# Performance work log

Measured on AMD Instinct MI355X. Metric: run time of the kernel, lower is better.

## Reference

```python
import jax, jax.numpy as jnp
import numpy as np

H, D, RPE_DIM, LAYERS = 8, 64, 64, 3
GAMMA = 0.999  # fixed decay (use_decay=True, requires_grad=False)
EPS = 1e-8

def simple_rmsnorm(x):
    # SimpleRMSNorm: x / (||x||_2 * d^{-1/2} + eps), no learned scale
    rms = jnp.sqrt(jnp.sum(x * x, axis=-1, keepdims=True)) * (x.shape[-1] ** -0.5)
    return x / (rms + EPS)

def rpe_transform(idx, pos_proj_w, pos_proj_b, layer_ws, layer_bs, out_w, out_b):
    # idx: (n, 1) -> (H, n, D)
    x = idx @ pos_proj_w + pos_proj_b            # (n, RPE_DIM)
    for i in range(LAYERS):                       # residual=False -> sequential
        x = jax.nn.relu(simple_rmsnorm(x)) @ layer_ws[i] + layer_bs[i]
    x = jax.nn.relu(simple_rmsnorm(x)) @ out_w + out_b   # (n, H*D)
    n = x.shape[0]
    return x.reshape(n, H, D).transpose(1, 0, 2)  # (H, n, D)

def setup_inputs() -> dict:
    key = jax.random.key(0)
    ks = jax.random.split(key, 6)
    b, n = 8, 4096
    s = RPE_DIM ** -0.5
    return {
        "x": jax.random.normal(ks[0], (b, H, n, D), jnp.float32),
        "pos_proj_w": jax.random.normal(ks[1], (1, RPE_DIM), jnp.float32),
        "pos_proj_b": jnp.zeros((RPE_DIM,), jnp.float32),
        "layer_ws": jax.random.normal(ks[2], (LAYERS, RPE_DIM, RPE_DIM), jnp.float32) * s,
        "layer_bs": jnp.zeros((LAYERS, RPE_DIM), jnp.float32),
        "out_w": jax.random.normal(ks[3], (RPE_DIM, H * D), jnp.float32) * s,
        "out_b": jnp.zeros((H * D,), jnp.float32),
    }

def reference(x, pos_proj_w, pos_proj_b, layer_ws, layer_bs, out_w, out_b):
    b, h, n, d = x.shape
    _rpe = lambda idx: rpe_transform(idx, pos_proj_w, pos_proj_b, layer_ws, layer_bs, out_w, out_b)
    # relative-position kernel values (par_type=1: raw integer offsets)
    zero = _rpe(jnp.zeros((1, 1), x.dtype))                       # (H, 1, D)
    pos_idx = jnp.arange(1, n, dtype=x.dtype).reshape(n - 1, 1)   # 1..n-1
    pos = _rpe(pos_idx)                                           # (H, n-1, D)
    neg = _rpe(-pos_idx[::-1])                                    # -(n-1)..-1
    # fixed exponential decay gamma^|offset|
    coef = jnp.arange(1, n, dtype=x.dtype).reshape(1, n - 1, 1)
    gamma = jnp.full((h, 1, d), GAMMA, x.dtype) ** coef           # (H, n-1, D)
    pos = gamma * pos
    neg = gamma[:, ::-1, :] * neg
    # act_type='none' -> identity activation on a
    a = jnp.concatenate([zero, pos, zero, neg], axis=1)           # (H, 2n, D)
    # circular conv of length 2n realizes the Toeplitz matvec
    y = jnp.fft.rfft(x, n=2 * n, axis=-2)                         # (b,H,n+1?,D) complex
    v = jnp.fft.rfft(a, n=2 * n, axis=-2)[None]                   # (1,H,.,D)
    out = jnp.fft.irfft(v * y, n=2 * n, axis=-2)[:, :, :n, :]
    return out
```

## Files before the change

kernel.cpp:

```cpp
#include <hip/hip_runtime.h>
#include <math.h>

#define NF 8192

__device__ __forceinline__ int phys(int e) { return e ^ (((e >> 4) & 7) << 1); }

__device__ __forceinline__ float2 cmul(float2 a, float2 b) {
    return make_float2(a.x*b.x - a.y*b.y, a.x*b.y + a.y*b.x);
}
__device__ __forceinline__ float2 cmulc(float2 a, float2 b) {
    return make_float2(a.x*b.x + a.y*b.y, a.y*b.x - a.x*b.y);
}
__device__ __forceinline__ float2 cadd(float2 a, float2 b){ return make_float2(a.x+b.x, a.y+b.y); }
__device__ __forceinline__ float2 csub(float2 a, float2 b){ return make_float2(a.x-b.x, a.y-b.y); }
__device__ __forceinline__ float2 mnegi(float2 a){ return make_float2(a.y, -a.x); }
__device__ __forceinline__ float2 mposi(float2 a){ return make_float2(-a.y, a.x); }
#define RSQ2 0.70710678118654752f
__device__ __forceinline__ float2 mw81 (float2 a){ return make_float2( RSQ2*(a.x+a.y),  RSQ2*(a.y-a.x)); }
__device__ __forceinline__ float2 mw83 (float2 a){ return make_float2( RSQ2*(a.y-a.x), -RSQ2*(a.x+a.y)); }
__device__ __forceinline__ float2 mw81c(float2 a){ return make_float2( RSQ2*(a.x-a.y),  RSQ2*(a.x+a.y)); }
__device__ __forceinline__ float2 mw83c(float2 a){ return make_float2(-RSQ2*(a.x+a.y),  RSQ2*(a.x-a.y)); }

#define C16_1 0.92387953251128674f
#define S16_1 0.38268343236508978f
#define C16_2 0.70710678118654752f

__device__ __forceinline__ float2 twbase(int ts) {
    float fa = (float)ts * (1.0f/8192.0f);
    return make_float2(__builtin_amdgcn_cosf(fa), -__builtin_amdgcn_sinf(fa));
}

__device__ __forceinline__ void dif8_core(float2& v0, float2& v1, float2& v2, float2& v3,
                                          float2& v4, float2& v5, float2& v6, float2& v7) {
    float2 t;
    t = csub(v0, v4); v0 = cadd(v0, v4); v4 = t;
    t = csub(v1, v5); v1 = cadd(v1, v5); v5 = mw81(t);
    t = csub(v2, v6); v2 = cadd(v2, v6); v6 = mnegi(t);
    t = csub(v3, v7); v3 = cadd(v3, v7); v7 = mw83(t);
    t = csub(v0, v2); v0 = cadd(v0, v2); v2 = t;
    t = csub(v1, v3); v1 = cadd(v1, v3); v3 = mnegi(t);
    t = csub(v4, v6); v4 = cadd(v4, v6); v6 = t;
    t = csub(v5, v7); v5 = cadd(v5, v7); v7 = mnegi(t);
    t = csub(v0, v1); v0 = cadd(v0, v1); v1 = t;
    t = csub(v2, v3); v2 = cadd(v2, v3); v3 = t;
    t = csub(v4, v5); v4 = cadd(v4, v5); v5 = t;
    t = csub(v6, v7); v6 = cadd(v6, v7); v7 = t;
}

__device__ __forceinline__ void dit8_core(float2& v0, float2& v1, float2& v2, float2& v3,
                                          float2& v4, float2& v5, float2& v6, float2& v7) {
    float2 t;
    t = csub(v0, v1); v0 = cadd(v0, v1); v1 = t;
    t = csub(v2, v3); v2 = cadd(v2, v3); v3 = t;
    t = csub(v4, v5); v4 = cadd(v4, v5); v5 = t;
    t = csub(v6, v7); v6 = cadd(v6, v7); v7 = t;
    t = v2;        v2 = csub(v0, t); v0 = cadd(v0, t);
    t = mposi(v3); v3 = csub(v1, t); v1 = cadd(v1, t);
    t = v6;        v6 = csub(v4, t); v4 = cadd(v4, t);
    t = mposi(v7); v7 = csub(v5, t); v5 = cadd(v5, t);
    t = v4;        v4 = csub(v0, t); v0 = cadd(v0, t);
    t = mw81c(v5); v5 = csub(v1, t); v1 = cadd(v1, t);
    t = mposi(v6); v6 = csub(v2, t); v2 = cadd(v2, t);
    t = mw83c(v7); v7 = csub(v3, t); v3 = cadd(v3, t);
}

#define TW_POWERS(ts) \
    float2 w1 = twbase(ts); \
    float2 w2 = cmul(w1, w1); \
    float2 w3 = cmul(w2, w1); \
    float2 w4 = cmul(w2, w2); \
    float2 w5 = cmul(w3, w2); \
    float2 w6 = cmul(w3, w3); \
    float2 w7 = cmul(w4, w3);

template<int M, int LM>
__device__ __forceinline__ void fwd8_lds(float2* Z, int tid) {
    #pragma unroll
    for (int q = 0; q < 2; ++q) {
        int beta = tid + q*512;
        int i    = beta & (M-1);
        int base = ((beta >> LM) << (LM+3)) + i;
        float2 v0 = Z[phys(base        )];
        float2 v1 = Z[phys(base + 1*M)];
        float2 v2 = Z[phys(base + 2*M)];
        float2 v3 = Z[phys(base + 3*M)];
        float2 v4 = Z[phys(base + 4*M)];
        float2 v5 = Z[phys(base + 5*M)];
        float2 v6 = Z[phys(base + 6*M)];
        float2 v7 = Z[phys(base + 7*M)];
        dif8_core(v0,v1,v2,v3,v4,v5,v6,v7);
        TW_POWERS((NF >> (LM+3)) * i)
        Z[phys(base        )] = v0;
        Z[phys(base + 4*M)] = cmul(v1, w4);
        Z[phys(base + 2*M)] = cmul(v2, w2);
        Z[phys(base + 6*M)] = cmul(v3, w6);
        Z[phys(base + 1*M)] = cmul(v4, w1);
        Z[phys(base + 5*M)] = cmul(v5, w5);
        Z[phys(base + 3*M)] = cmul(v6, w3);
        Z[phys(base + 7*M)] = cmul(v7, w7);
    }
}

template<int M, int LM>
__device__ __forceinline__ void inv8_lds(float2* Z, int tid) {
    #pragma unroll
    for (int q = 0; q < 2; ++q) {
        int beta = tid + q*512;
        int i    = beta & (M-1);
        int base = ((beta >> LM) << (LM+3)) + i;
        TW_POWERS((NF >> (LM+3)) * i)
        float2 v0 = Z[phys(base        )];
        float2 v1 = cmulc(Z[phys(base + 4*M)], w4);
        float2 v2 = cmulc(Z[phys(base + 2*M)], w2);
        float2 v3 = cmulc(Z[phys(base + 6*M)], w6);
        float2 v4 = cmulc(Z[phys(base + 1*M)], w1);
        float2 v5 = cmulc(Z[phys(base + 5*M)], w5);
        float2 v6 = cmulc(Z[phys(base + 3*M)], w3);
        float2 v7 = cmulc(Z[phys(base + 7*M)], w7);
        dit8_core(v0,v1,v2,v3,v4,v5,v6,v7);
        Z[phys(base        )] = v0;
        Z[phys(base + 1*M)] = v1;
        Z[phys(base + 2*M)] = v2;
        Z[phys(base + 3*M)] = v3;
        Z[phys(base + 4*M)] = v4;
        Z[phys(base + 5*M)] = v5;
        Z[phys(base + 6*M)] = v6;
        Z[phys(base + 7*M)] = v7;
    }
}


__global__ __launch_bounds__(512) void rpe_kernel(
    const float* __restrict__ pw,  const float* __restrict__ pb,
    const float* __restrict__ lws, const float* __restrict__ lbs,
    const float* __restrict__ ow,  const float* __restrict__ ob,
    float* __restrict__ a_buf)
{
    __shared__ float sW[3][64][64];
    __shared__ float sWo[64][64];
    __shared__ float sB[3][64];
    __shared__ float sPW[64], sPB[64];
    __shared__ float sAct[8][4][64];
    int tid = threadIdx.x;
    for (int idx = tid; idx < 3*64*64; idx += 512) ((float*)sW)[idx] = lws[idx];
    if (tid < 192) ((float*)sB)[tid] = lbs[tid];
    if (tid < 64) { sPW[tid] = pw[tid]; sPB[tid] = pb[tid]; }
    __syncthreads();

    int wv = tid >> 6, lane = tid & 63;
    int e0 = blockIdx.x * 32 + wv * 4;
    float dec[4];
    #pragma unroll
    for (int s = 0; s < 4; ++s) {
        int e = e0 + s;
        float p = (e == 4096) ? 0.f : ((e < 4096) ? (float)e : (float)(e - 8192));
        int m = (e < 4096) ? e : (8192 - e);
        if (e == 4096) m = 0;
        dec[s] = exp2f(-0.0014434309482562475f * (float)m);

        float xv = fmaf(p, sPW[lane], sPB[lane]);
        #pragma unroll
        for (int L = 0; L < 3; ++L) {
            float ss = xv * xv;
            #pragma unroll
            for (int o = 1; o < 64; o <<= 1) ss += __shfl_xor(ss, o);
            sAct[wv][s][lane] = fmaxf(xv / (sqrtf(ss) * 0.125f + 1e-8f), 0.f);
            float y = sB[L][lane];
            const float4* av = reinterpret_cast<const float4*>(sAct[wv][s]);
            #pragma unroll
            for (int k = 0; k < 16; ++k) {
                float4 a4 = av[k];
                y = fmaf(a4.x, sW[L][4*k  ][lane], y);
                y = fmaf(a4.y, sW[L][4*k+1][lane], y);
                y = fmaf(a4.z, sW[L][4*k+2][lane], y);
                y = fmaf(a4.w, sW[L][4*k+3][lane], y);
            }
            xv = y;
        }
        float ss = xv * xv;
        #pragma unroll
        for (int o = 1; o < 64; o <<= 1) ss += __shfl_xor(ss, o);
        sAct[wv][s][lane] = fmaxf(xv / (sqrtf(ss) * 0.125f + 1e-8f), 0.f);
    }
    for (int qq = 0; qq < 8; ++qq) {
        __syncthreads();
        for (int idx = tid; idx < 4096; idx += 512)
            ((float*)sWo)[idx] = ow[(size_t)(idx >> 6)*512 + qq*64 + (idx & 63)];
        __syncthreads();
        #pragma unroll
        for (int s = 0; s < 4; ++s) {
            float y = ob[qq*64 + lane];
            const float4* av = reinterpret_cast<const float4*>(sAct[wv][s]);
            #pragma unroll
            for (int k = 0; k < 16; ++k) {
                float4 a4 = av[k];
                y = fmaf(a4.x, sWo[4*k  ][lane], y);
                y = fmaf(a4.y, sWo[4*k+1][lane], y);
                y = fmaf(a4.z, sWo[4*k+2][lane], y);
                y = fmaf(a4.w, sWo[4*k+3][lane], y);
            }
            a_buf[(size_t)(qq*64 + lane)*NF + (e0 + s)] = y * dec[s];
        }
    }
}

__global__ __launch_bounds__(512, 4) void afft_kernel(
    const float* __restrict__ a_buf, float2* __restrict__ Afft)
{
    __shared__ __align__(16) float2 Z[NF];
    int cc = blockIdx.x, tid = threadIdx.x;
    const float* col = a_buf + (size_t)cc * NF;
    #pragma unroll
    for (int q = 0; q < 2; ++q) {
        int i = tid + q*512;
        float2 v0 = make_float2(col[i       ], 0.f);
        float2 v1 = make_float2(col[i + 1024], 0.f);
        float2 v2 = make_float2(col[i + 2048], 0.f);
        float2 v3 = make_float2(col[i + 3072], 0.f);
        float2 v4 = make_float2(col[i + 4096], 0.f);
        float2 v5 = make_float2(col[i + 5120], 0.f);
        float2 v6 = make_float2(col[i + 6144], 0.f);
        float2 v7 = make_float2(col[i + 7168], 0.f);
        dif8_core(v0,v1,v2,v3,v4,v5,v6,v7);
        TW_POWERS(i)
        Z[phys(i        )] = v0;
        Z[phys(i + 4096)] = cmul(v1, w4);
        Z[phys(i + 2048)] = cmul(v2, w2);
        Z[phys(i + 6144)] = cmul(v3, w6);
        Z[phys(i + 1024)] = cmul(v4, w1);
        Z[phys(i + 5120)] = cmul(v5, w5);
        Z[phys(i + 3072)] = cmul(v6, w3);
        Z[phys(i + 7168)] = cmul(v7, w7);
    }
    __syncthreads();
    fwd8_lds<128, 7>(Z, tid);  __syncthreads();
    fwd8_lds<16,  4>(Z, tid);  __syncthreads();
    {
        int c = tid, sw4 = c & 7;
        float4* Z4 = reinterpret_cast<float4*>(Z);
        float4* oc4 = reinterpret_cast<float4*>(Afft + (size_t)cc * NF);
        float2 z[16];
        #pragma unroll
        for (int j = 0; j < 8; ++j) {
            float4 wv = Z4[c*8 + (j ^ sw4)];
            z[2*j]   = make_float2(wv.x, wv.y);
            z[2*j+1] = make_float2(wv.z, wv.w);
        }
        dif8_core(z[0],z[2],z[4],z[6],z[8],z[10],z[12],z[14]);
        dif8_core(z[1],z[3],z[5],z[7],z[9],z[11],z[13],z[15]);
        #define A4K(k, ZE, ZO, WR, WI) { \
            float2 w = make_float2((WR)*(ZO).x - (WI)*(ZO).y, (WR)*(ZO).y + (WI)*(ZO).x); \
            float2 pp = cadd(ZE, w), rr = csub(ZE, w); \
            oc4[(k)*512 + c] = make_float4(pp.x, pp.y, rr.x, rr.y); }
        { float2 pp = cadd(z[0], z[1]), rr = csub(z[0], z[1]);
          oc4[0*512 + c] = make_float4(pp.x, pp.y, rr.x, rr.y); }
        A4K(1, z[8],  z[9],   C16_1, -S16_1)
        A4K(2, z[4],  z[5],   C16_2, -C16_2)
        A4K(3, z[12], z[13],  S16_1, -C16_1)
        { float2 w = mnegi(z[3]);
          float2 pp = cadd(z[2], w), rr = csub(z[2], w);
          oc4[4*512 + c] = make_float4(pp.x, pp.y, rr.x, rr.y); }
        A4K(5, z[10], z[11], -S16_1, -C16_1)
        A4K(6, z[6],  z[7],  -C16_2, -C16_2)
        A4K(7, z[14], z[15], -C16_1, -S16_1)
        #undef A4K
    }
}

__global__ __launch_bounds__(512, 4) void conv_kernel(
    const float* __restrict__ x, const float2* __restrict__ Afft,
    float* __restrict__ out)
{
    __shared__ __align__(16) float2 Z[NF];
    int blk = blockIdx.x;
    int c8 = blk & 7, r = blk >> 3;
    int d  = ((c8 & 1) << 5) | (r & 31);
    int h  = (((r >> 5) & 3) << 1) | ((c8 >> 1) & 1);
    int bp = (((r >> 7) & 1) << 1) | ((c8 >> 2) & 1);
    int tid = threadIdx.x;
    size_t base0 = ((size_t)((bp*2 + 0)*8 + h) * 4096) * 64 + d;
    size_t base1 = ((size_t)((bp*2 + 1)*8 + h) * 4096) * 64 + d;

    #pragma unroll
    for (int q = 0; q < 2; ++q) {
        int i = tid + q*512;
        float2 v0 = make_float2(x[base0 + (size_t)(i       )*64], x[base1 + (size_t)(i       )*64]);
        float2 v1 = make_float2(x[base0 + (size_t)(i + 1024)*64], x[base1 + (size_t)(i + 1024)*64]);
        float2 v2 = make_float2(x[base0 + (size_t)(i + 2048)*64], x[base1 + (size_t)(i + 2048)*64]);
        float2 v3 = make_float2(x[base0 + (size_t)(i + 3072)*64], x[base1 + (size_t)(i + 3072)*64]);
        float2 v4 = v0;
        float2 v5 = mw81(v1);
        float2 v6 = mnegi(v2);
        float2 v7 = mw83(v3);
        float2 t;
        t = csub(v0, v2); v0 = cadd(v0, v2); v2 = t;
        t = csub(v1, v3); v1 = cadd(v1, v3); v3 = mnegi(t);
        t = csub(v4, v6); v4 = cadd(v4, v6); v6 = t;
        t = csub(v5, v7); v5 = cadd(v5, v7); v7 = mnegi(t);
        t = csub(v0, v1); v0 = cadd(v0, v1); v1 = t;
        t = csub(v2, v3); v2 = cadd(v2, v3); v3 = t;
        t = csub(v4, v5); v4 = cadd(v4, v5); v5 = t;
        t = csub(v6, v7); v6 = cadd(v6, v7); v7 = t;
        TW_POWERS(i)
        Z[phys(i        )] = v0;
        Z[phys(i + 4096)] = cmul(v1, w4);
        Z[phys(i + 2048)] = cmul(v2, w2);
        Z[phys(i + 6144)] = cmul(v3, w6);
        Z[phys(i + 1024)] = cmul(v4, w1);
        Z[phys(i + 5120)] = cmul(v5, w5);
        Z[phys(i + 3072)] = cmul(v6, w3);
        Z[phys(i + 7168)] = cmul(v7, w7);
    }
    __syncthreads();
    fwd8_lds<128, 7>(Z, tid);  __syncthreads();
    fwd8_lds<16,  4>(Z, tid);  __syncthreads();

    {
        int c = tid, sw4 = c & 7;
        float4* Z4 = reinterpret_cast<float4*>(Z);
        const float4* A4 = reinterpret_cast<const float4*>(Afft + (size_t)(h*64 + d)*NF);
        float2 z[16];
        #pragma unroll
        for (int j = 0; j < 8; ++j) {
            float4 wv = Z4[c*8 + (j ^ sw4)];
            z[2*j]   = make_float2(wv.x, wv.y);
            z[2*j+1] = make_float2(wv.z, wv.w);
        }
        dif8_core(z[0],z[2],z[4],z[6],z[8],z[10],z[12],z[14]);
        dif8_core(z[1],z[3],z[5],z[7],z[9],z[11],z[13],z[15]);
        #define P4K(k, ZE, ZO, WR, WI) { \
            float2 w = make_float2((WR)*(ZO).x - (WI)*(ZO).y, (WR)*(ZO).y + (WI)*(ZO).x); \
            float2 pp = cadd(ZE, w), rr = csub(ZE, w); \
            float4 av = A4[(k)*512 + c]; \
            pp = cmul(pp, make_float2(av.x, av.y)); \
            rr = cmul(rr, make_float2(av.z, av.w)); \
            ZE = cadd(pp, rr); \
            ZO = csub(pp, rr); }
        { float2 pp = cadd(z[0], z[1]), rr = csub(z[0], z[1]);
          float4 av = A4[0*512 + c];
          pp = cmul(pp, make_float2(av.x, av.y));
          rr = cmul(rr, make_float2(av.z, av.w));
          z[0] = cadd(pp, rr); z[1] = csub(pp, rr); }
        P4K(1, z[8],  z[9],   C16_1, -S16_1)
        P4K(2, z[4],  z[5],   C16_2, -C16_2)
        P4K(3, z[12], z[13],  S16_1, -C16_1)
        { float2 w = mnegi(z[3]);
          float2 pp = cadd(z[2], w), rr = csub(z[2], w);
          float4 av = A4[4*512 + c];
          pp = cmul(pp, make_float2(av.x, av.y));
          rr = cmul(rr, make_float2(av.z, av.w));
          z[2] = cadd(pp, rr); z[3] = csub(pp, rr); }
        P4K(5, z[10], z[11], -S16_1, -C16_1)
        P4K(6, z[6],  z[7],  -C16_2, -C16_2)
        P4K(7, z[14], z[15], -C16_1, -S16_1)
        #undef P4K
        z[3]  = mposi(z[3]);
        z[5]  = cmul(z[5],  make_float2( C16_2,  C16_2));
        z[7]  = cmul(z[7],  make_float2(-C16_2,  C16_2));
        z[9]  = cmul(z[9],  make_float2( C16_1,  S16_1));
        z[11] = cmul(z[11], make_float2(-S16_1,  C16_1));
        z[13] = cmul(z[13], make_float2( S16_1,  C16_1));
        z[15] = cmul(z[15], make_float2(-C16_1,  S16_1));
        dit8_core(z[0],z[2],z[4],z[6],z[8],z[10],z[12],z[14]);
        dit8_core(z[1],z[3],z[5],z[7],z[9],z[11],z[13],z[15]);
        #pragma unroll
        for (int j = 0; j < 8; ++j)
            Z4[c*8 + (j ^ sw4)] = make_float4(z[2*j].x, z[2*j].y, z[2*j+1].x, z[2*j+1].y);
    }
    __syncthreads();
    inv8_lds<16,  4>(Z, tid);  __syncthreads();
    inv8_lds<128, 7>(Z, tid);  __syncthreads();

    const float sc = 1.0f/8192.0f;
    #pragma unroll
    for (int q = 0; q < 2; ++q) {
        int i = tid + q*512;
        TW_POWERS(i)
        float2 v0 = Z[phys(i        )];
        float2 v1 = cmulc(Z[phys(i + 4096)], w4);
        float2 v2 = cmulc(Z[phys(i + 2048)], w2);
        float2 v3 = cmulc(Z[phys(i + 6144)], w6);
        float2 v4 = cmulc(Z[phys(i + 1024)], w1);
        float2 v5 = cmulc(Z[phys(i + 5120)], w5);
        float2 v6 = cmulc(Z[phys(i + 3072)], w3);
        float2 v7 = cmulc(Z[phys(i + 7168)], w7);
        float2 t;
        t = csub(v0, v1); v0 = cadd(v0, v1); v1 = t;
        t = csub(v2, v3); v2 = cadd(v2, v3); v3 = t;
        t = csub(v4, v5); v4 = cadd(v4, v5); v5 = t;
        t = csub(v6, v7); v6 = cadd(v6, v7); v7 = t;
        t = v2;        v2 = csub(v0, t); v0 = cadd(v0, t);
        t = mposi(v3); v3 = csub(v1, t); v1 = cadd(v1, t);
        t = v6;        v6 = csub(v4, t); v4 = cadd(v4, t);
        t = mposi(v7); v7 = csub(v5, t); v5 = cadd(v5, t);
        v0 = cadd(v0, v4);
        v1 = cadd(v1, mw81c(v5));
        v2 = cadd(v2, mposi(v6));
        v3 = cadd(v3, mw83c(v7));
        out[base0 + (size_t)(i       )*64] = v0.x * sc;
        out[base1 + (size_t)(i       )*64] = v0.y * sc;
        out[base0 + (size_t)(i + 1024)*64] = v1.x * sc;
        out[base1 + (size_t)(i + 1024)*64] = v1.y * sc;
        out[base0 + (size_t)(i + 2048)*64] = v2.x * sc;
        out[base1 + (size_t)(i + 2048)*64] = v2.y * sc;
        out[base0 + (size_t)(i + 3072)*64] = v3.x * sc;
        out[base1 + (size_t)(i + 3072)*64] = v3.y * sc;
    }
}

extern "C" void kernel_launch(void* const* d_in, const int* in_sizes, int n_in,
                              void* d_out, int out_size, void* d_ws, size_t ws_size,
                              hipStream_t stream) {
    const float* x   = (const float*)d_in[0];
    const float* pw  = (const float*)d_in[1];
    const float* pb  = (const float*)d_in[2];
    const float* lws = (const float*)d_in[3];
    const float* lbs = (const float*)d_in[4];
    const float* ow  = (const float*)d_in[5];
    const float* ob  = (const float*)d_in[6];
    float* out = (float*)d_out;
    char* ws = (char*)d_ws;
    float*  a_buf = (float*)ws;
    float2* Afft  = (float2*)(ws + (size_t)512*NF*4);

    rpe_kernel<<<256, 512, 0, stream>>>(pw, pb, lws, lbs, ow, ob, a_buf);
    afft_kernel<<<512, 512, 0, stream>>>(a_buf, Afft);
    conv_kernel<<<2048, 512, 0, stream>>>(x, Afft, out);
}
```

Baseline: 543.2 us.

## Process two d-columns per conv block with float2 loads; interleave RPE weights

The conv kernel now handles two adjacent d columns per block. It loads and stores x/out as float2 pairs and runs the FFT convolution twice through a shared device function, with half as many blocks. The RPE kernel stores its weights pair-interleaved in LDS for float2 reads, processes two positions per wave instead of four, and launches twice as many blocks. The goal is better global memory coalescing on the strided x/out accesses and more parallelism in the RPE stage, at the cost of more registers and less per-block parallelism in conv.

```diff
diff --git a/kernel.cpp b/kernel.cpp
--- a/kernel.cpp
+++ b/kernel.cpp
@@ -129,165 +129,16 @@
     }
 }
 
-
-__global__ __launch_bounds__(512) void rpe_kernel(
-    const float* __restrict__ pw,  const float* __restrict__ pb,
-    const float* __restrict__ lws, const float* __restrict__ lbs,
-    const float* __restrict__ ow,  const float* __restrict__ ob,
-    float* __restrict__ a_buf)
+__device__ __forceinline__ void fft8192_conv(float2* Z, int tid, const float4* __restrict__ A4,
+                                             const float2 (&vin)[8], float2 (&vout)[8])
 {
-    __shared__ float sW[3][64][64];
-    __shared__ float sWo[64][64];
-    __shared__ float sB[3][64];
-    __shared__ float sPW[64], sPB[64];
-    __shared__ float sAct[8][4][64];
-    int tid = threadIdx.x;
-    for (int idx = tid; idx < 3*64*64; idx += 512) ((float*)sW)[idx] = lws[idx];
-    if (tid < 192) ((float*)sB)[tid] = lbs[tid];
-    if (tid < 64) { sPW[tid] = pw[tid]; sPB[tid] = pb[tid]; }
-    __syncthreads();
-
-    int wv = tid >> 6, lane = tid & 63;
-    int e0 = blockIdx.x * 32 + wv * 4;
-    float dec[4];
-    #pragma unroll
-    for (int s = 0; s < 4; ++s) {
-        int e = e0 + s;
-        float p = (e == 4096) ? 0.f : ((e < 4096) ? (float)e : (float)(e - 8192));
-        int m = (e < 4096) ? e : (8192 - e);
-        if (e == 4096) m = 0;
-        dec[s] = exp2f(-0.0014434309482562475f * (float)m);
-
-        float xv = fmaf(p, sPW[lane], sPB[lane]);
-        #pragma unroll
-        for (int L = 0; L < 3; ++L) {
-            float ss = xv * xv;
-            #pragma unroll
-            for (int o = 1; o < 64; o <<= 1) ss += __shfl_xor(ss, o);
-            sAct[wv][s][lane] = fmaxf(xv / (sqrtf(ss) * 0.125f + 1e-8f), 0.f);
-            float y = sB[L][lane];
-            const float4* av = reinterpret_cast<const float4*>(sAct[wv][s]);
-            #pragma unroll
-            for (int k = 0; k < 16; ++k) {
-                float4 a4 = av[k];
-                y = fmaf(a4.x, sW[L][4*k  ][lane], y);
-                y = fmaf(a4.y, sW[L][4*k+1][lane], y);
-                y = fmaf(a4.z, sW[L][4*k+2][lane], y);
-                y = fmaf(a4.w, sW[L][4*k+3][lane], y);
-            }
-            xv = y;
-        }
-        float ss = xv * xv;
-        #pragma unroll
-        for (int o = 1; o < 64; o <<= 1) ss += __shfl_xor(ss, o);
-        sAct[wv][s][lane] = fmaxf(xv / (sqrtf(ss) * 0.125f + 1e-8f), 0.f);
-    }
-    for (int qq = 0; qq < 8; ++qq) {
-        __syncthreads();
-        for (int idx = tid; idx < 4096; idx += 512)
-            ((float*)sWo)[idx] = ow[(size_t)(idx >> 6)*512 + qq*64 + (idx & 63)];
-        __syncthreads();
-        #pragma unroll
-        for (int s = 0; s < 4; ++s) {
-            float y = ob[qq*64 + lane];
-            const float4* av = reinterpret_cast<const float4*>(sAct[wv][s]);
-            #pragma unroll
-            for (int k = 0; k < 16; ++k) {
-                float4 a4 = av[k];
-                y = fmaf(a4.x, sWo[4*k  ][lane], y);
-                y = fmaf(a4.y, sWo[4*k+1][lane], y);
-                y = fmaf(a4.z, sWo[4*k+2][lane], y);
-                y = fmaf(a4.w, sWo[4*k+3][lane], y);
-            }
-            a_buf[(size_t)(qq*64 + lane)*NF + (e0 + s)] = y * dec[s];
-        }
-    }
-}
-
-__global__ __launch_bounds__(512, 4) void afft_kernel(
-    const float* __restrict__ a_buf, float2* __restrict__ Afft)
-{
-    __shared__ __align__(16) float2 Z[NF];
-    int cc = blockIdx.x, tid = threadIdx.x;
-    const float* col = a_buf + (size_t)cc * NF;
     #pragma unroll
     for (int q = 0; q < 2; ++q) {
         int i = tid + q*512;
-        float2 v0 = make_float2(col[i       ], 0.f);
-        float2 v1 = make_float2(col[i + 1024], 0.f);
-        float2 v2 = make_float2(col[i + 2048], 0.f);
-        float2 v3 = make_float2(col[i + 3072], 0.f);
-        float2 v4 = make_float2(col[i + 4096], 0.f);
-        float2 v5 = make_float2(col[i + 5120], 0.f);
-        float2 v6 = make_float2(col[i + 6144], 0.f);
-        float2 v7 = make_float2(col[i + 7168], 0.f);
-        dif8_core(v0,v1,v2,v3,v4,v5,v6,v7);
-        TW_POWERS(i)
-        Z[phys(i        )] = v0;
-        Z[phys(i + 4096)] = cmul(v1, w4);
-        Z[phys(i + 2048)] = cmul(v2, w2);
-        Z[phys(i + 6144)] = cmul(v3, w6);
-        Z[phys(i + 1024)] = cmul(v4, w1);
-        Z[phys(i + 5120)] = cmul(v5, w5);
-        Z[phys(i + 3072)] = cmul(v6, w3);
-        Z[phys(i + 7168)] = cmul(v7, w7);
-    }
-    __syncthreads();
-    fwd8_lds<128, 7>(Z, tid);  __syncthreads();
-    fwd8_lds<16,  4>(Z, tid);  __syncthreads();
-    {
-        int c = tid, sw4 = c & 7;
-        float4* Z4 = reinterpret_cast<float4*>(Z);
-        float4* oc4 = reinterpret_cast<float4*>(Afft + (size_t)cc * NF);
-        float2 z[16];
-        #pragma unroll
-        for (int j = 0; j < 8; ++j) {
-            float4 wv = Z4[c*8 + (j ^ sw4)];
-            z[2*j]   = make_float2(wv.x, wv.y);
-            z[2*j+1] = make_float2(wv.z, wv.w);
-        }
-        dif8_core(z[0],z[2],z[4],z[6],z[8],z[10],z[12],z[14]);
-        dif8_core(z[1],z[3],z[5],z[7],z[9],z[11],z[13],z[15]);
-        #define A4K(k, ZE, ZO, WR, WI) { \
-            float2 w = make_float2((WR)*(ZO).x - (WI)*(ZO).y, (WR)*(ZO).y + (WI)*(ZO).x); \
-            float2 pp = cadd(ZE, w), rr = csub(ZE, w); \
-            oc4[(k)*512 + c] = make_float4(pp.x, pp.y, rr.x, rr.y); }
-        { float2 pp = cadd(z[0], z[1]), rr = csub(z[0], z[1]);
-          oc4[0*512 + c] = make_float4(pp.x, pp.y, rr.x, rr.y); }
-        A4K(1, z[8],  z[9],   C16_1, -S16_1)
-        A4K(2, z[4],  z[5],   C16_2, -C16_2)
-        A4K(3, z[12], z[13],  S16_1, -C16_1)
-        { float2 w = mnegi(z[3]);
-          float2 pp = cadd(z[2], w), rr = csub(z[2], w);
-          oc4[4*512 + c] = make_float4(pp.x, pp.y, rr.x, rr.y); }
-        A4K(5, z[10], z[11], -S16_1, -C16_1)
-        A4K(6, z[6],  z[7],  -C16_2, -C16_2)
-        A4K(7, z[14], z[15], -C16_1, -S16_1)
-        #undef A4K
-    }
-}
-
-__global__ __launch_bounds__(512, 4) void conv_kernel(
-    const float* __restrict__ x, const float2* __restrict__ Afft,
-    float* __restrict__ out)
-{
-    __shared__ __align__(16) float2 Z[NF];
-    int blk = blockIdx.x;
-    int c8 = blk & 7, r = blk >> 3;
-    int d  = ((c8 & 1) << 5) | (r & 31);
-    int h  = (((r >> 5) & 3) << 1) | ((c8 >> 1) & 1);
-    int bp = (((r >> 7) & 1) << 1) | ((c8 >> 2) & 1);
-    int tid = threadIdx.x;
-    size_t base0 = ((size_t)((bp*2 + 0)*8 + h) * 4096) * 64 + d;
-    size_t base1 = ((size_t)((bp*2 + 1)*8 + h) * 4096) * 64 + d;
-
-    #pragma unroll
-    for (int q = 0; q < 2; ++q) {
-        int i = tid + q*512;
-        float2 v0 = make_float2(x[base0 + (size_t)(i       )*64], x[base1 + (size_t)(i       )*64]);
-        float2 v1 = make_float2(x[base0 + (size_t)(i + 1024)*64], x[base1 + (size_t)(i + 1024)*64]);
-        float2 v2 = make_float2(x[base0 + (size_t)(i + 2048)*64], x[base1 + (size_t)(i + 2048)*64]);
-        float2 v3 = make_float2(x[base0 + (size_t)(i + 3072)*64], x[base1 + (size_t)(i + 3072)*64]);
+        float2 v0 = vin[q*4+0];
+        float2 v1 = vin[q*4+1];
+        float2 v2 = vin[q*4+2];
+        float2 v3 = vin[q*4+3];
         float2 v4 = v0;
         float2 v5 = mw81(v1);
         float2 v6 = mnegi(v2);
@@ -318,7 +169,6 @@
     {
         int c = tid, sw4 = c & 7;
         float4* Z4 = reinterpret_cast<float4*>(Z);
-        const float4* A4 = reinterpret_cast<const float4*>(Afft + (size_t)(h*64 + d)*NF);
         float2 z[16];
         #pragma unroll
         for (int j = 0; j < 8; ++j) {
@@ -371,7 +221,6 @@
     inv8_lds<16,  4>(Z, tid);  __syncthreads();
     inv8_lds<128, 7>(Z, tid);  __syncthreads();
 
-    const float sc = 1.0f/8192.0f;
     #pragma unroll
     for (int q = 0; q < 2; ++q) {
         int i = tid + q*512;
@@ -393,18 +242,209 @@
         t = mposi(v3); v3 = csub(v1, t); v1 = cadd(v1, t);
         t = v6;        v6 = csub(v4, t); v4 = cadd(v4, t);
         t = mposi(v7); v7 = csub(v5, t); v5 = cadd(v5, t);
-        v0 = cadd(v0, v4);
-        v1 = cadd(v1, mw81c(v5));
-        v2 = cadd(v2, mposi(v6));
-        v3 = cadd(v3, mw83c(v7));
-        out[base0 + (size_t)(i       )*64] = v0.x * sc;
-        out[base1 + (size_t)(i       )*64] = v0.y * sc;
-        out[base0 + (size_t)(i + 1024)*64] = v1.x * sc;
-        out[base1 + (size_t)(i + 1024)*64] = v1.y * sc;
-        out[base0 + (size_t)(i + 2048)*64] = v2.x * sc;
-        out[base1 + (size_t)(i + 2048)*64] = v2.y * sc;
-        out[base0 + (size_t)(i + 3072)*64] = v3.x * sc;
-        out[base1 + (size_t)(i + 3072)*64] = v3.y * sc;
+        vout[q*4+0] = cadd(v0, v4);
+        vout[q*4+1] = cadd(v1, mw81c(v5));
+        vout[q*4+2] = cadd(v2, mposi(v6));
+        vout[q*4+3] = cadd(v3, mw83c(v7));
+    }
+}
+
+
+__global__ __launch_bounds__(512) void rpe_kernel(
+    const float* __restrict__ pw,  const float* __restrict__ pb,
+    const float* __restrict__ lws, const float* __restrict__ lbs,
+    const float* __restrict__ ow,  const float* __restrict__ ob,
+    float* __restrict__ a_buf)
+{
+    __shared__ float sW2[3][32][64][2];
+    __shared__ float sWo2[32][64][2];
+    __shared__ float sB[3][64];
+    __shared__ float sPW[64], sPB[64];
+    __shared__ float sAct[8][2][64];
+    int tid = threadIdx.x;
+    for (int idx = tid; idx < 3*64*64; idx += 512) {
+        int L = idx >> 12, rem = idx & 4095, k = rem >> 6, c = rem & 63;
+        sW2[L][k >> 1][c][k & 1] = lws[idx];
+    }
+    if (tid < 192) ((float*)sB)[tid] = lbs[tid];
+    if (tid < 64) { sPW[tid] = pw[tid]; sPB[tid] = pb[tid]; }
+    __syncthreads();
+
+    int wv = tid >> 6, lane = tid & 63;
+    int e0 = blockIdx.x * 16 + wv * 2;
+    float xv[2], dec[2];
+    #pragma unroll
+    for (int s = 0; s < 2; ++s) {
+        int e = e0 + s;
+        float p = (e == 4096) ? 0.f : ((e < 4096) ? (float)e : (float)(e - 8192));
+        int m = (e < 4096) ? e : (8192 - e);
+        if (e == 4096) m = 0;
+        dec[s] = exp2f(-0.0014434309482562475f * (float)m);
+        xv[s] = fmaf(p, sPW[lane], sPB[lane]);
+    }
+
+    #pragma unroll
+    for (int L = 0; L < 3; ++L) {
+        #pragma unroll
+        for (int s = 0; s < 2; ++s) {
+            float v = xv[s];
+            float ss = v * v;
+            #pragma unroll
+            for (int o = 1; o < 64; o <<= 1) ss += __shfl_xor(ss, o);
+            sAct[wv][s][lane] = fmaxf(v / (sqrtf(ss) * 0.125f + 1e-8f), 0.f);
+            float y = sB[L][lane];
+            const float2* ap = reinterpret_cast<const float2*>(sAct[wv][s]);
+            const float2* wp = reinterpret_cast<const float2*>(sW2[L]);
+            #pragma unroll
+            for (int kk = 0; kk < 32; ++kk) {
+                float2 a2 = ap[kk];
+                float2 ww = wp[kk*64 + lane];
+                y = fmaf(a2.x, ww.x, y);
+                y = fmaf(a2.y, ww.y, y);
+            }
+            xv[s] = y;
+        }
+    }
+    #pragma unroll
+    for (int s = 0; s < 2; ++s) {
+        float v = xv[s];
+        float ss = v * v;
+        #pragma unroll
+        for (int o = 1; o < 64; o <<= 1) ss += __shfl_xor(ss, o);
+        sAct[wv][s][lane] = fmaxf(v / (sqrtf(ss) * 0.125f + 1e-8f), 0.f);
+    }
+    for (int qq = 0; qq < 8; ++qq) {
+        __syncthreads();
+        for (int idx = tid; idx < 4096; idx += 512) {
+            int k = idx >> 6, c = idx & 63;
+            sWo2[k >> 1][c][k & 1] = ow[(size_t)k*512 + qq*64 + c];
+        }
+        __syncthreads();
+        #pragma unroll
+        for (int s = 0; s < 2; ++s) {
+            float y = ob[qq*64 + lane];
+            const float2* ap = reinterpret_cast<const float2*>(sAct[wv][s]);
+            const float2* wp = reinterpret_cast<const float2*>(sWo2);
+            #pragma unroll
+            for (int kk = 0; kk < 32; ++kk) {
+                float2 a2 = ap[kk];
+                float2 ww = wp[kk*64 + lane];
+                y = fmaf(a2.x, ww.x, y);
+                y = fmaf(a2.y, ww.y, y);
+            }
+            a_buf[(size_t)(qq*64 + lane)*NF + (e0 + s)] = y * dec[s];
+        }
+    }
+}
+
+__global__ __launch_bounds__(512, 4) void afft_kernel(
+    const float* __restrict__ a_buf, float2* __restrict__ Afft)
+{
+    __shared__ __align__(16) float2 Z[NF];
+    int cc = blockIdx.x, tid = threadIdx.x;
+    const float* col = a_buf + (size_t)cc * NF;
+    #pragma unroll
+    for (int q = 0; q < 2; ++q) {
+        int i = tid + q*512;
+        float2 v0 = make_float2(col[i       ], 0.f);
+        float2 v1 = make_float2(col[i + 1024], 0.f);
+        float2 v2 = make_float2(col[i + 2048], 0.f);
+        float2 v3 = make_float2(col[i + 3072], 0.f);
+        float2 v4 = make_float2(col[i + 4096], 0.f);
+        float2 v5 = make_float2(col[i + 5120], 0.f);
+        float2 v6 = make_float2(col[i + 6144], 0.f);
+        float2 v7 = make_float2(col[i + 7168], 0.f);
+        dif8_core(v0,v1,v2,v3,v4,v5,v6,v7);
+        TW_POWERS(i)
+        Z[phys(i        )] = v0;
+        Z[phys(i + 4096)] = cmul(v1, w4);
+        Z[phys(i + 2048)] = cmul(v2, w2);
+        Z[phys(i + 6144)] = cmul(v3, w6);
+        Z[phys(i + 1024)] = cmul(v4, w1);
+        Z[phys(i + 5120)] = cmul(v5, w5);
+        Z[phys(i + 3072)] = cmul(v6, w3);
+        Z[phys(i + 7168)] = cmul(v7, w7);
+    }
+    __syncthreads();
+    fwd8_lds<128, 7>(Z, tid);  __syncthreads();
+    fwd8_lds<16,  4>(Z, tid);  __syncthreads();
+    {
+        int c = tid, sw4 = c & 7;
+        float4* Z4 = reinterpret_cast<float4*>(Z);
+        float4* oc4 = reinterpret_cast<float4*>(Afft + (size_t)cc * NF);
+        float2 z[16];
+        #pragma unroll
+        for (int j = 0; j < 8; ++j) {
+            float4 wv = Z4[c*8 + (j ^ sw4)];
+            z[2*j]   = make_float2(wv.x, wv.y);
+            z[2*j+1] = make_float2(wv.z, wv.w);
+        }
+        dif8_core(z[0],z[2],z[4],z[6],z[8],z[10],z[12],z[14]);
+        dif8_core(z[1],z[3],z[5],z[7],z[9],z[11],z[13],z[15]);
+        #define A4K(k, ZE, ZO, WR, WI) { \
+            float2 w = make_float2((WR)*(ZO).x - (WI)*(ZO).y, (WR)*(ZO).y + (WI)*(ZO).x); \
+            float2 pp = cadd(ZE, w), rr = csub(ZE, w); \
+            oc4[(k)*512 + c] = make_float4(pp.x, pp.y, rr.x, rr.y); }
+        { float2 pp = cadd(z[0], z[1]), rr = csub(z[0], z[1]);
+          oc4[0*512 + c] = make_float4(pp.x, pp.y, rr.x, rr.y); }
+        A4K(1, z[8],  z[9],   C16_1, -S16_1)
+        A4K(2, z[4],  z[5],   C16_2, -C16_2)
+        A4K(3, z[12], z[13],  S16_1, -C16_1)
+        { float2 w = mnegi(z[3]);
+          float2 pp = cadd(z[2], w), rr = csub(z[2], w);
+          oc4[4*512 + c] = make_float4(pp.x, pp.y, rr.x, rr.y); }
+        A4K(5, z[10], z[11], -S16_1, -C16_1)
+        A4K(6, z[6],  z[7],  -C16_2, -C16_2)
+        A4K(7, z[14], z[15], -C16_1, -S16_1)
+        #undef A4K
+    }
+}
+
+__global__ __launch_bounds__(512, 4) void conv_kernel(
+    const float* __restrict__ x, const float2* __restrict__ Afft,
+    float* __restrict__ out)
+{
+    __shared__ __align__(16) float2 Z[NF];
+    int blk = blockIdx.x;
+    int c8 = blk & 7, r = blk >> 3;
+    int dp = ((c8 & 1) << 4) | (r & 15);
+    int h  = (((r >> 4) & 3) << 1) | ((c8 >> 1) & 1);
+    int bp = (((r >> 6) & 1) << 1) | ((c8 >> 2) & 1);
+    int d  = dp * 2;
+    int tid = threadIdx.x;
+    size_t base0 = ((size_t)((bp*2 + 0)*8 + h) * 4096) * 64 + d;
+    size_t base1 = ((size_t)((bp*2 + 1)*8 + h) * 4096) * 64 + d;
+
+    float2 inA[8], inB[8];
+    #pragma unroll
+    for (int q = 0; q < 2; ++q) {
+        #pragma unroll
+        for (int l = 0; l < 4; ++l) {
+            int p = tid + q*512 + l*1024;
+            float2 f0 = *reinterpret_cast<const float2*>(&x[base0 + (size_t)p*64]);
+            float2 f1 = *reinterpret_cast<const float2*>(&x[base1 + (size_t)p*64]);
+            inA[q*4+l] = make_float2(f0.x, f1.x);
+            inB[q*4+l] = make_float2(f0.y, f1.y);
+        }
+    }
+
+    const float4* A4a = reinterpret_cast<const float4*>(Afft + (size_t)(h*64 + d    )*NF);
+    const float4* A4b = reinterpret_cast<const float4*>(Afft + (size_t)(h*64 + d + 1)*NF);
+    float2 outA[8], outB[8];
+    fft8192_conv(Z, tid, A4a, inA, outA);
+    __syncthreads();
+    fft8192_conv(Z, tid, A4b, inB, outB);
+
+    const float sc = 1.0f/8192.0f;
+    #pragma unroll
+    for (int q = 0; q < 2; ++q) {
+        #pragma unroll
+        for (int l = 0; l < 4; ++l) {
+            int p = tid + q*512 + l*1024;
+            float2 yA = outA[q*4+l], yB = outB[q*4+l];
+            *reinterpret_cast<float2*>(&out[base0 + (size_t)p*64]) = make_float2(yA.x * sc, yB.x * sc);
+            *reinterpret_cast<float2*>(&out[base1 + (size_t)p*64]) = make_float2(yA.y * sc, yB.y * sc);
+        }
     }
 }
 
@@ -423,7 +463,7 @@
     float*  a_buf = (float*)ws;
     float2* Afft  = (float2*)(ws + (size_t)512*NF*4);
 
-    rpe_kernel<<<256, 512, 0, stream>>>(pw, pb, lws, lbs, ow, ob, a_buf);
+    rpe_kernel<<<512, 512, 0, stream>>>(pw, pb, lws, lbs, ow, ob, a_buf);
     afft_kernel<<<512, 512, 0, stream>>>(a_buf, Afft);
-    conv_kernel<<<2048, 512, 0, stream>>>(x, Afft, out);
-}
+    conv_kernel<<<1024, 512, 0, stream>>>(x, Afft, out);
+}
```

New measurement: 616.1 us. 13.4% more time.
